# Kernel optimization log

Measured on AMD Instinct MI355X. Metric: run time of the kernel, lower is better.

The kernel has to match this reference:

```python
import jax, jax.numpy as jnp
import numpy as np

IN_FEATURES = 1024
OUT_FEATURES = 1024
NUM_GRIDS = 8
GRID_MIN, GRID_MAX = -2.0, 2.0
DENOM = (GRID_MAX - GRID_MIN) / (NUM_GRIDS - 1)
LN_EPS = 1e-5
GRID = jnp.linspace(GRID_MIN, GRID_MAX, NUM_GRIDS)


def setup_inputs() -> dict:
    key = jax.random.key(0)
    k_x, k_sw, k_bw = jax.random.split(key, 3)
    N = 8192
    x = jax.random.normal(k_x, (N, IN_FEATURES), dtype=jnp.float32)
    ln_gamma = jnp.ones((IN_FEATURES,), dtype=jnp.float32)
    ln_beta = jnp.zeros((IN_FEATURES,), dtype=jnp.float32)
    # trunc_normal(std=0.1) approximated by scaled normal
    spline_w = 0.1 * jax.random.normal(k_sw, (OUT_FEATURES, IN_FEATURES * NUM_GRIDS), dtype=jnp.float32)
    base_w = jax.random.normal(k_bw, (OUT_FEATURES, IN_FEATURES), dtype=jnp.float32) * (1.0 / np.sqrt(IN_FEATURES))
    base_b = jnp.zeros((OUT_FEATURES,), dtype=jnp.float32)
    return {"x": x, "ln_gamma": ln_gamma, "ln_beta": ln_beta,
            "spline_w": spline_w, "base_w": base_w, "base_b": base_b}


def reference(x, ln_gamma, ln_beta, spline_w, base_w, base_b):
    # LayerNorm over last dim
    mu = jnp.mean(x, axis=-1, keepdims=True)
    var = jnp.var(x, axis=-1, keepdims=True)
    xn = (x - mu) * jax.lax.rsqrt(var + LN_EPS) * ln_gamma + ln_beta
    # RBF basis: [N, in, G]
    basis = jnp.exp(-jnp.square((xn[..., None] - GRID) / DENOM))
    basis = basis.reshape(x.shape[0], IN_FEATURES * NUM_GRIDS)
    y = jnp.einsum('nk,ok->no', basis, spline_w)
    y = y + jnp.einsum('nd,od->no', jax.nn.silu(x), base_w) + base_b
    return y
```

## Files before the change

kernel.cpp:

```cpp
#include <hip/hip_runtime.h>
#include <hip/hip_bf16.h>
#include <stdint.h>

#define IN_F 1024
#define OUT_F 1024
#define NG 8
#define KSPLINE 8192
#define KDIM 9216
#define KHALF 4608
#define M_ROWS 8192
#define LOG2E 1.4426950408889634f
#define KC 2.1019642153762872f

#define A_BLOCKS (M_ROWS / 4)
#define W_BLOCKS ((OUT_F * 2304) / 256)
#define RB (KDIM * 2)

using half4v = __attribute__((ext_vector_type(4))) _Float16;
using half8  = __attribute__((ext_vector_type(8))) _Float16;
using f32x4  = __attribute__((ext_vector_type(4))) float;

#define AS1 __attribute__((address_space(1)))
#define AS3 __attribute__((address_space(3)))

__global__ __launch_bounds__(256) void prep_kernel(
        const float* __restrict__ x, const float* __restrict__ gamma,
        const float* __restrict__ beta, const float* __restrict__ sw,
        const float* __restrict__ bw, _Float16* __restrict__ A,
        _Float16* __restrict__ W) {
    if (blockIdx.x >= A_BLOCKS) {
        int idx = (blockIdx.x - A_BLOCKS) * 256 + threadIdx.x;
        int o   = idx / 2304;
        int k4  = idx - o * 2304;
        f32x4 v;
        if (k4 < 2048) v = __builtin_nontemporal_load(&((const f32x4*)sw)[(size_t)o * 2048 + k4]);
        else           v = __builtin_nontemporal_load(&((const f32x4*)bw)[(size_t)o * 256 + (k4 - 2048)]);
        half4v h = { (_Float16)v.x, (_Float16)v.y, (_Float16)v.z, (_Float16)v.w };
        *(half4v*)(W + (size_t)idx * 4) = h;
        return;
    }
    const int wave = threadIdx.x >> 6, lane = threadIdx.x & 63;
    const int row = blockIdx.x * 4 + wave;
    const float* xr = x + (size_t)row * IN_F;

    float xv[16];
    float s = 0.0f, s2 = 0.0f;
#pragma unroll
    for (int j = 0; j < 16; ++j) {
        float v = __builtin_nontemporal_load(&xr[j * 64 + lane]);
        xv[j] = v;
        s += v;
        s2 += v * v;
    }
#pragma unroll
    for (int off = 32; off > 0; off >>= 1) {
        s  += __shfl_xor(s, off);
        s2 += __shfl_xor(s2, off);
    }
    float mu   = s * (1.0f / IN_F);
    float var  = s2 * (1.0f / IN_F) - mu * mu;
    float rstd = rsqrtf(var + 1e-5f);

    const float cq[8] = {
        -2.0000000f * KC, -1.4285715f * KC, -0.8571429f * KC, -0.2857143f * KC,
         0.2857143f * KC,  0.8571429f * KC,  1.4285715f * KC,  2.0000000f * KC };

    _Float16* Arow = A + (size_t)row * KDIM;
    half8* basis_out = (half8*)Arow;
    _Float16* silu_out = Arow + KSPLINE;
#pragma unroll
    for (int j = 0; j < 16; ++j) {
        int f = j * 64 + lane;
        float xs = xv[j];
        float xq = ((xs - mu) * rstd * gamma[f] + beta[f]) * KC;
        half8 h;
#pragma unroll
        for (int g = 0; g < 8; ++g) {
            float v = xq - cq[g];
            h[g] = (_Float16)exp2f(-(v * v));
        }
        __builtin_nontemporal_store(h, &basis_out[f]);
        __builtin_nontemporal_store((_Float16)(xs / (1.0f + exp2f(-xs * LOG2E))), &silu_out[f]);
    }
}

__global__ __launch_bounds__(512, 2) void gemm_kernel(
        const _Float16* __restrict__ A, const _Float16* __restrict__ W,
        const float* __restrict__ bias, float* __restrict__ C,
        float* __restrict__ P, int ntiles, int gpz) {
    extern __shared__ __align__(16) char smem[];
    const int tid  = threadIdx.x;
    const int wave = tid >> 6, lane = tid & 63;
    const int wm = wave >> 2, wn = wave & 3;

    const int lb = blockIdx.x;
    const int per_xcd = gridDim.x >> 5;
    const int xcd = lb & 7, sl = lb >> 3;
    const int g  = xcd * per_xcd + (sl >> 2);
    const int bn = sl & 3;
    const int bm = g / gpz;
    const int z  = g - bm * gpz;

    const int l8 = lane >> 3;
    const int chunkswz = ((lane & 7) ^ l8) << 4;
    const size_t zoff = (size_t)z * (KHALF * 2);
    const int gA[4] = {0, 128, 64, 192};
    const int gB[4] = {0, 128, 32, 160};
    const char* pA[4];
    const char* pB[4];
#pragma unroll
    for (int s = 0; s < 4; ++s) {
        pA[s] = (const char*)A + (size_t)(bm * 256 + gA[s] + wave * 8 + l8) * RB
                + zoff + chunkswz;
        pB[s] = (const char*)W + (size_t)(bn * 256 + gB[s] + (wave >> 2) * 64
                + (wave & 3) * 8 + l8) * RB + zoff + chunkswz;
    }

#define STAGE_A(s, nb, colb) __builtin_amdgcn_global_load_lds( \
        (const AS1 void*)(pA[s] + (colb)), \
        (AS3 void*)(smem + (nb) + (s) * 8192 + wave * 1024), 16, 0, 0)
#define STAGE_B(s, nb, colb) __builtin_amdgcn_global_load_lds( \
        (const AS1 void*)(pB[s] + (colb)), \
        (AS3 void*)(smem + (nb) + 32768 + (s) * 8192 + wave * 1024), 16, 0, 0)

    const int lm  = lane & 15;
    const int hi  = (lane >> 4) << 4;
    const int swz = (lm & 7) << 4;
    const int ck0 = (0  + hi) ^ swz;
    const int ck1 = (64 + hi) ^ swz;
    const int aB0 = (0 + wm) * 8192 + lm * 128;
    const int aB1 = (2 + wm) * 8192 + lm * 128;
    const int bB0 = 32768 + (0 + (wn >> 1)) * 8192 + ((wn & 1) * 32 + lm) * 128;
    const int bB1 = 32768 + (2 + (wn >> 1)) * 8192 + ((wn & 1) * 32 + lm) * 128;

    f32x4 acc[8][4] = {};

    STAGE_A(0, 0, 0); STAGE_A(1, 0, 0);
    STAGE_B(0, 0, 0); STAGE_B(1, 0, 0);
    STAGE_B(2, 0, 0); STAGE_B(3, 0, 0);
    STAGE_A(2, 0, 0); STAGE_A(3, 0, 0);
    asm volatile("s_waitcnt vmcnt(4)" ::: "memory");
    __builtin_amdgcn_s_barrier();

    for (int kt = 0; kt < ntiles; ++kt) {
        const int cb = (kt & 1) * 65536;
        const int nb = cb ^ 65536;
        const size_t col = (size_t)(kt + 1) * 128;
        const bool pref = (kt + 1 < ntiles);

        half8 aF[4][2], bF[2][2];
#pragma unroll
        for (int m = 0; m < 4; ++m) {
            aF[m][0] = *(const half8*)(smem + cb + aB0 + m * 2048 + ck0);
            aF[m][1] = *(const half8*)(smem + cb + aB0 + m * 2048 + ck1);
        }
#pragma unroll
        for (int n = 0; n < 2; ++n) {
            bF[n][0] = *(const half8*)(smem + cb + bB0 + n * 2048 + ck0);
            bF[n][1] = *(const half8*)(smem + cb + bB0 + n * 2048 + ck1);
        }
        asm volatile("s_waitcnt vmcnt(2)" ::: "memory");
        if (pref) { STAGE_A(0, nb, col); STAGE_A(1, nb, col); }
        asm volatile("s_waitcnt lgkmcnt(8)" ::: "memory");
        __builtin_amdgcn_s_barrier();
        asm volatile("s_waitcnt lgkmcnt(0)" ::: "memory");
        __builtin_amdgcn_s_setprio(1);
#pragma unroll
        for (int n = 0; n < 2; ++n)
#pragma unroll
            for (int m = 0; m < 4; ++m)
                acc[m][n] = __builtin_amdgcn_mfma_f32_16x16x32_f16(aF[m][0], bF[n][0], acc[m][n], 0, 0, 0);
#pragma unroll
        for (int n = 0; n < 2; ++n)
#pragma unroll
            for (int m = 0; m < 4; ++m)
                acc[m][n] = __builtin_amdgcn_mfma_f32_16x16x32_f16(aF[m][1], bF[n][1], acc[m][n], 0, 0, 0);
        __builtin_amdgcn_s_setprio(0);
        __builtin_amdgcn_s_barrier();

        half8 bG[2][2];
#pragma unroll
        for (int n = 0; n < 2; ++n) {
            bG[n][0] = *(const half8*)(smem + cb + bB1 + n * 2048 + ck0);
            bG[n][1] = *(const half8*)(smem + cb + bB1 + n * 2048 + ck1);
        }
        if (pref) {
            asm volatile("s_waitcnt vmcnt(2)" ::: "memory");
            STAGE_B(0, nb, col); STAGE_B(1, nb, col);
        } else {
            asm volatile("s_waitcnt vmcnt(0)" ::: "memory");
        }
        __builtin_amdgcn_s_barrier();
        asm volatile("s_waitcnt lgkmcnt(0)" ::: "memory");
        __builtin_amdgcn_s_setprio(1);
#pragma unroll
        for (int n = 0; n < 2; ++n)
#pragma unroll
            for (int m = 0; m < 4; ++m)
                acc[m][2 + n] = __builtin_amdgcn_mfma_f32_16x16x32_f16(aF[m][0], bG[n][0], acc[m][2 + n], 0, 0, 0);
#pragma unroll
        for (int n = 0; n < 2; ++n)
#pragma unroll
            for (int m = 0; m < 4; ++m)
                acc[m][2 + n] = __builtin_amdgcn_mfma_f32_16x16x32_f16(aF[m][1], bG[n][1], acc[m][2 + n], 0, 0, 0);
        __builtin_amdgcn_s_setprio(0);
        __builtin_amdgcn_s_barrier();

        half8 aG[4][2];
#pragma unroll
        for (int m = 0; m < 4; ++m) {
            aG[m][0] = *(const half8*)(smem + cb + aB1 + m * 2048 + ck0);
            aG[m][1] = *(const half8*)(smem + cb + aB1 + m * 2048 + ck1);
        }
        if (pref) { STAGE_B(2, nb, col); STAGE_B(3, nb, col); }
        __builtin_amdgcn_s_barrier();
        asm volatile("s_waitcnt lgkmcnt(0)" ::: "memory");
        __builtin_amdgcn_s_setprio(1);
#pragma unroll
        for (int n = 0; n < 2; ++n)
#pragma unroll
            for (int m = 0; m < 4; ++m)
                acc[4 + m][n] = __builtin_amdgcn_mfma_f32_16x16x32_f16(aG[m][0], bF[n][0], acc[4 + m][n], 0, 0, 0);
#pragma unroll
        for (int n = 0; n < 2; ++n)
#pragma unroll
            for (int m = 0; m < 4; ++m)
                acc[4 + m][n] = __builtin_amdgcn_mfma_f32_16x16x32_f16(aG[m][1], bF[n][1], acc[4 + m][n], 0, 0, 0);
        __builtin_amdgcn_s_setprio(0);
        __builtin_amdgcn_s_barrier();

        if (pref) {
            asm volatile("s_waitcnt vmcnt(2)" ::: "memory");
            STAGE_A(2, nb, col); STAGE_A(3, nb, col);
        }
        __builtin_amdgcn_s_barrier();
        __builtin_amdgcn_s_setprio(1);
#pragma unroll
        for (int n = 0; n < 2; ++n)
#pragma unroll
            for (int m = 0; m < 4; ++m)
                acc[4 + m][2 + n] = __builtin_amdgcn_mfma_f32_16x16x32_f16(aG[m][0], bG[n][0], acc[4 + m][2 + n], 0, 0, 0);
#pragma unroll
        for (int n = 0; n < 2; ++n)
#pragma unroll
            for (int m = 0; m < 4; ++m)
                acc[4 + m][2 + n] = __builtin_amdgcn_mfma_f32_16x16x32_f16(aG[m][1], bG[n][1], acc[4 + m][2 + n], 0, 0, 0);
        __builtin_amdgcn_s_setprio(0);
        __builtin_amdgcn_s_barrier();
    }

    const int cn  = lane & 15;
    const int rm4 = (lane >> 4) * 4;
    float* dst = z ? P : C;
#pragma unroll
    for (int nf = 0; nf < 4; ++nf) {
        int col = bn * 256 + wn * 64 + nf * 16 + cn;
        float bv = z ? 0.0f : bias[col];
#pragma unroll
        for (int mf = 0; mf < 8; ++mf) {
            int row = bm * 256 + wm * 128 + mf * 16 + rm4;
            float* cp = dst + (size_t)row * OUT_F + col;
#pragma unroll
            for (int r = 0; r < 4; ++r)
                cp[(size_t)r * OUT_F] = acc[mf][nf][r] + bv;
        }
    }
}

__global__ __launch_bounds__(256) void reduce_kernel(float* __restrict__ C,
        const float* __restrict__ P) {
    const int n4 = M_ROWS * OUT_F / 4;
    float4* c4 = (float4*)C;
    const float4* p4 = (const float4*)P;
    for (int i = blockIdx.x * 256 + threadIdx.x; i < n4; i += 2048 * 256) {
        float4 a = c4[i];
        float4 b = p4[i];
        a.x += b.x; a.y += b.y; a.z += b.z; a.w += b.w;
        c4[i] = a;
    }
}

extern "C" void kernel_launch(void* const* d_in, const int* in_sizes, int n_in,
                              void* d_out, int out_size, void* d_ws, size_t ws_size,
                              hipStream_t stream) {
    const float* x     = (const float*)d_in[0];
    const float* gamma = (const float*)d_in[1];
    const float* beta  = (const float*)d_in[2];
    const float* sw    = (const float*)d_in[3];
    const float* bw    = (const float*)d_in[4];
    const float* bb    = (const float*)d_in[5];
    float* out = (float*)d_out;

    char* ws = (char*)d_ws;
    size_t offW = 0;
    size_t offA = (size_t)OUT_F * KDIM * 2;
    size_t offP = offA + (size_t)M_ROWS * KDIM * 2;
    size_t need = offP + (size_t)M_ROWS * OUT_F * 4;
    _Float16* Wb = (_Float16*)(ws + offW);
    _Float16* Ab = (_Float16*)(ws + offA);
    float*    Pb = (float*)(ws + offP);
    const int split = (ws_size >= need);

    static int s_attr = 0;
    if (!s_attr) {
        (void)hipFuncSetAttribute(reinterpret_cast<const void*>(gemm_kernel),
                            hipFuncAttributeMaxDynamicSharedMemorySize, 131072);
        s_attr = 1;
    }

    prep_kernel<<<A_BLOCKS + W_BLOCKS, 256, 0, stream>>>(
        x, gamma, beta, sw, bw, Ab, Wb);
    if (split) {
        gemm_kernel<<<256, 512, 131072, stream>>>(Ab, Wb, bb, out, Pb, KHALF / 64, 2);
        reduce_kernel<<<2048, 256, 0, stream>>>(out, Pb);
    } else {
        gemm_kernel<<<128, 512, 131072, stream>>>(Ab, Wb, bb, out, Pb, KDIM / 64, 1);
    }
}
```

Before: 287.5 us.

## Fuse RBF basis generation into GEMM, staging only per-row stats and SiLU

Instead of materializing the 8192x9216 fp16 basis+SiLU matrix in the prep kernel, prep now writes only fp16 SiLU values and per-row mean/rstd. The GEMM kernel computes the eight RBF basis values on the fly from x for the spline K-range and writes them directly into LDS, while still streaming SiLU tiles via global_load_lds for the tail K-range. This removes roughly 150 MB of global write+read traffic for the basis matrix, at the cost of extra exp2 ALU work and fp32 x loads inside the GEMM main loop, and slightly more LDS for gamma/beta.

```diff
diff --git a/kernel.cpp b/kernel.cpp
--- a/kernel.cpp
+++ b/kernel.cpp
@@ -15,19 +15,20 @@
 #define A_BLOCKS (M_ROWS / 4)
 #define W_BLOCKS ((OUT_F * 2304) / 256)
 #define RB (KDIM * 2)
+#define GBOFF 131072
 
 using half4v = __attribute__((ext_vector_type(4))) _Float16;
 using half8  = __attribute__((ext_vector_type(8))) _Float16;
 using f32x4  = __attribute__((ext_vector_type(4))) float;
+using f32x2  = __attribute__((ext_vector_type(2))) float;
 
 #define AS1 __attribute__((address_space(1)))
 #define AS3 __attribute__((address_space(3)))
 
 __global__ __launch_bounds__(256) void prep_kernel(
-        const float* __restrict__ x, const float* __restrict__ gamma,
-        const float* __restrict__ beta, const float* __restrict__ sw,
-        const float* __restrict__ bw, _Float16* __restrict__ A,
-        _Float16* __restrict__ W) {
+        const float* __restrict__ x, const float* __restrict__ sw,
+        const float* __restrict__ bw, _Float16* __restrict__ S,
+        float* __restrict__ musig, _Float16* __restrict__ W) {
     if (blockIdx.x >= A_BLOCKS) {
         int idx = (blockIdx.x - A_BLOCKS) * 256 + threadIdx.x;
         int o   = idx / 2304;
@@ -47,7 +48,7 @@
     float s = 0.0f, s2 = 0.0f;
 #pragma unroll
     for (int j = 0; j < 16; ++j) {
-        float v = __builtin_nontemporal_load(&xr[j * 64 + lane]);
+        float v = xr[j * 64 + lane];
         xv[j] = v;
         s += v;
         s2 += v * v;
@@ -60,32 +61,36 @@
     float mu   = s * (1.0f / IN_F);
     float var  = s2 * (1.0f / IN_F) - mu * mu;
     float rstd = rsqrtf(var + 1e-5f);
-
-    const float cq[8] = {
+    if (lane == 0) {
+        f32x2 ms; ms[0] = mu; ms[1] = rstd;
+        ((f32x2*)musig)[row] = ms;
+    }
+    _Float16* Srow = S + (size_t)row * IN_F;
+#pragma unroll
+    for (int j = 0; j < 16; ++j) {
+        float xs = xv[j];
+        Srow[j * 64 + lane] = (_Float16)(xs / (1.0f + exp2f(-xs * LOG2E)));
+    }
+}
+
+__device__ __forceinline__ half8 spline8(float xv, float mu, float rs, float gk, float bk) {
+    const float cqg[8] = {
         -2.0000000f * KC, -1.4285715f * KC, -0.8571429f * KC, -0.2857143f * KC,
          0.2857143f * KC,  0.8571429f * KC,  1.4285715f * KC,  2.0000000f * KC };
-
-    _Float16* Arow = A + (size_t)row * KDIM;
-    half8* basis_out = (half8*)Arow;
-    _Float16* silu_out = Arow + KSPLINE;
-#pragma unroll
-    for (int j = 0; j < 16; ++j) {
-        int f = j * 64 + lane;
-        float xs = xv[j];
-        float xq = ((xs - mu) * rstd * gamma[f] + beta[f]) * KC;
-        half8 h;
-#pragma unroll
-        for (int g = 0; g < 8; ++g) {
-            float v = xq - cq[g];
-            h[g] = (_Float16)exp2f(-(v * v));
-        }
-        __builtin_nontemporal_store(h, &basis_out[f]);
-        __builtin_nontemporal_store((_Float16)(xs / (1.0f + exp2f(-xs * LOG2E))), &silu_out[f]);
-    }
+    float xq = fmaf((xv - mu) * rs, gk, bk);
+    half8 h;
+#pragma unroll
+    for (int g = 0; g < 8; ++g) {
+        float d = xq - cqg[g];
+        h[g] = (_Float16)__builtin_amdgcn_exp2f(-(d * d));
+    }
+    return h;
 }
 
 __global__ __launch_bounds__(512, 2) void gemm_kernel(
-        const _Float16* __restrict__ A, const _Float16* __restrict__ W,
+        const _Float16* __restrict__ W, const _Float16* __restrict__ S,
+        const float* __restrict__ x, const float* __restrict__ musig,
+        const float* __restrict__ gamma, const float* __restrict__ beta,
         const float* __restrict__ bias, float* __restrict__ C,
         float* __restrict__ P, int ntiles, int gpz) {
     extern __shared__ __align__(16) char smem[];
@@ -100,28 +105,40 @@
     const int bn = sl & 3;
     const int bm = g / gpz;
     const int z  = g - bm * gpz;
+    const int ksoff = z * KHALF;
 
     const int l8 = lane >> 3;
     const int chunkswz = ((lane & 7) ^ l8) << 4;
-    const size_t zoff = (size_t)z * (KHALF * 2);
-    const int gA[4] = {0, 128, 64, 192};
-    const int gB[4] = {0, 128, 32, 160};
-    const char* pA[4];
+    const int gAr[4] = {0, 128, 64, 192};
+    const int gB[4]  = {0, 128, 32, 160};
     const char* pB[4];
+    const char* pS[4];
+    const float* xp[4];
 #pragma unroll
     for (int s = 0; s < 4; ++s) {
-        pA[s] = (const char*)A + (size_t)(bm * 256 + gA[s] + wave * 8 + l8) * RB
-                + zoff + chunkswz;
         pB[s] = (const char*)W + (size_t)(bn * 256 + gB[s] + (wave >> 2) * 64
-                + (wave & 3) * 8 + l8) * RB + zoff + chunkswz;
-    }
-
-#define STAGE_A(s, nb, colb) __builtin_amdgcn_global_load_lds( \
-        (const AS1 void*)(pA[s] + (colb)), \
-        (AS3 void*)(smem + (nb) + (s) * 8192 + wave * 1024), 16, 0, 0)
+                + (wave & 3) * 8 + l8) * RB + (size_t)ksoff * 2 + chunkswz;
+        int arow = bm * 256 + gAr[s] + wave * 8 + l8;
+        pS[s] = (const char*)S + (size_t)arow * (IN_F * 2) + chunkswz;
+    }
+    const int r6 = tid >> 3;
+    const int c8 = tid & 7;
+    const int wAbase = r6 * 128 + ((c8 ^ (r6 & 7)) << 4);
+    float mu4[4], rs4[4];
+#pragma unroll
+    for (int s = 0; s < 4; ++s) {
+        int arow = bm * 256 + gAr[s] + r6;
+        xp[s] = x + (size_t)arow * IN_F;
+        f32x2 ms = ((const f32x2*)musig)[arow];
+        mu4[s] = ms[0]; rs4[s] = ms[1];
+    }
+
 #define STAGE_B(s, nb, colb) __builtin_amdgcn_global_load_lds( \
         (const AS1 void*)(pB[s] + (colb)), \
         (AS3 void*)(smem + (nb) + 32768 + (s) * 8192 + wave * 1024), 16, 0, 0)
+#define STAGE_S(s, nb, colb) __builtin_amdgcn_global_load_lds( \
+        (const AS1 void*)(pS[s] + (colb)), \
+        (AS3 void*)(smem + (nb) + (s) * 8192 + wave * 1024), 16, 0, 0)
 
     const int lm  = lane & 15;
     const int hi  = (lane >> 4) << 4;
@@ -135,19 +152,68 @@
 
     f32x4 acc[8][4] = {};
 
-    STAGE_A(0, 0, 0); STAGE_A(1, 0, 0);
-    STAGE_B(0, 0, 0); STAGE_B(1, 0, 0);
-    STAGE_B(2, 0, 0); STAGE_B(3, 0, 0);
-    STAGE_A(2, 0, 0); STAGE_A(3, 0, 0);
-    asm volatile("s_waitcnt vmcnt(4)" ::: "memory");
+#define MFMA_QUAD(MB, NB2, Aa, Bb)                                              \
+    __builtin_amdgcn_s_barrier();                                               \
+    asm volatile("s_waitcnt lgkmcnt(0)" ::: "memory");                          \
+    __builtin_amdgcn_sched_barrier(0);                                          \
+    __builtin_amdgcn_s_setprio(1);                                              \
+    _Pragma("unroll")                                                           \
+    for (int n = 0; n < 2; ++n)                                                 \
+        _Pragma("unroll")                                                       \
+        for (int m = 0; m < 4; ++m)                                             \
+            acc[(MB)+m][(NB2)+n] = __builtin_amdgcn_mfma_f32_16x16x32_f16(      \
+                Aa[m][0], Bb[n][0], acc[(MB)+m][(NB2)+n], 0, 0, 0);             \
+    _Pragma("unroll")                                                           \
+    for (int n = 0; n < 2; ++n)                                                 \
+        _Pragma("unroll")                                                       \
+        for (int m = 0; m < 4; ++m)                                             \
+            acc[(MB)+m][(NB2)+n] = __builtin_amdgcn_mfma_f32_16x16x32_f16(      \
+                Aa[m][1], Bb[n][1], acc[(MB)+m][(NB2)+n], 0, 0, 0);             \
+    __builtin_amdgcn_s_setprio(0);                                              \
+    __builtin_amdgcn_s_barrier();
+
+    {
+        f32x2 t0; t0[0] = gamma[tid] * KC;       t0[1] = beta[tid] * KC;
+        f32x2 t1; t1[0] = gamma[tid + 512] * KC; t1[1] = beta[tid + 512] * KC;
+        *(f32x2*)(smem + GBOFF + tid * 8) = t0;
+        *(f32x2*)(smem + GBOFF + (tid + 512) * 8) = t1;
+    }
+    const int f00 = z * 576 + c8;
+    float xf0[4];
+#pragma unroll
+    for (int s = 0; s < 4; ++s) xf0[s] = xp[s][f00];
+    STAGE_B(0, 0, 0); STAGE_B(1, 0, 0); STAGE_B(2, 0, 0); STAGE_B(3, 0, 0);
+    __syncthreads();
+    {
+        f32x2 gb0 = *(const f32x2*)(smem + GBOFF + f00 * 8);
+#pragma unroll
+        for (int s = 0; s < 4; ++s) {
+            half8 h = spline8(xf0[s], mu4[s], rs4[s], gb0[0], gb0[1]);
+            *(half8*)(smem + s * 8192 + wAbase) = h;
+        }
+    }
+    asm volatile("s_waitcnt lgkmcnt(0)" ::: "memory");
     __builtin_amdgcn_s_barrier();
 
     for (int kt = 0; kt < ntiles; ++kt) {
         const int cb = (kt & 1) * 65536;
         const int nb = cb ^ 65536;
-        const size_t col = (size_t)(kt + 1) * 128;
         const bool pref = (kt + 1 < ntiles);
-
+        const int nk = ksoff + (kt + 1) * 64;
+        const bool nsil = nk >= KSPLINE;
+        const size_t bcolb = (size_t)(kt + 1) * 128;
+        const int fb = z * 576 + (kt + 1) * 8 + c8;
+        size_t scolb = 0;
+        if (nsil) scolb = (size_t)(nk - KSPLINE) * 2;
+
+        float xf[4];
+        if (pref) {
+            if (nsil) { STAGE_S(0, nb, scolb); STAGE_S(1, nb, scolb); }
+            else {
+#pragma unroll
+                for (int s = 0; s < 4; ++s) xf[s] = xp[s][fb];
+            }
+        }
         half8 aF[4][2], bF[2][2];
 #pragma unroll
         for (int m = 0; m < 4; ++m) {
@@ -159,24 +225,14 @@
             bF[n][0] = *(const half8*)(smem + cb + bB0 + n * 2048 + ck0);
             bF[n][1] = *(const half8*)(smem + cb + bB0 + n * 2048 + ck1);
         }
-        asm volatile("s_waitcnt vmcnt(2)" ::: "memory");
-        if (pref) { STAGE_A(0, nb, col); STAGE_A(1, nb, col); }
+        if (pref) {
+            if (nsil) asm volatile("s_waitcnt vmcnt(2)" ::: "memory");
+            else      asm volatile("s_waitcnt vmcnt(4)" ::: "memory");
+        } else {
+            asm volatile("s_waitcnt vmcnt(0)" ::: "memory");
+        }
         asm volatile("s_waitcnt lgkmcnt(8)" ::: "memory");
-        __builtin_amdgcn_s_barrier();
-        asm volatile("s_waitcnt lgkmcnt(0)" ::: "memory");
-        __builtin_amdgcn_s_setprio(1);
-#pragma unroll
-        for (int n = 0; n < 2; ++n)
-#pragma unroll
-            for (int m = 0; m < 4; ++m)
-                acc[m][n] = __builtin_amdgcn_mfma_f32_16x16x32_f16(aF[m][0], bF[n][0], acc[m][n], 0, 0, 0);
-#pragma unroll
-        for (int n = 0; n < 2; ++n)
-#pragma unroll
-            for (int m = 0; m < 4; ++m)
-                acc[m][n] = __builtin_amdgcn_mfma_f32_16x16x32_f16(aF[m][1], bF[n][1], acc[m][n], 0, 0, 0);
-        __builtin_amdgcn_s_setprio(0);
-        __builtin_amdgcn_s_barrier();
+        MFMA_QUAD(0, 0, aF, bF)
 
         half8 bG[2][2];
 #pragma unroll
@@ -184,27 +240,8 @@
             bG[n][0] = *(const half8*)(smem + cb + bB1 + n * 2048 + ck0);
             bG[n][1] = *(const half8*)(smem + cb + bB1 + n * 2048 + ck1);
         }
-        if (pref) {
-            asm volatile("s_waitcnt vmcnt(2)" ::: "memory");
-            STAGE_B(0, nb, col); STAGE_B(1, nb, col);
-        } else {
-            asm volatile("s_waitcnt vmcnt(0)" ::: "memory");
-        }
-        __builtin_amdgcn_s_barrier();
-        asm volatile("s_waitcnt lgkmcnt(0)" ::: "memory");
-        __builtin_amdgcn_s_setprio(1);
-#pragma unroll
-        for (int n = 0; n < 2; ++n)
-#pragma unroll
-            for (int m = 0; m < 4; ++m)
-                acc[m][2 + n] = __builtin_amdgcn_mfma_f32_16x16x32_f16(aF[m][0], bG[n][0], acc[m][2 + n], 0, 0, 0);
-#pragma unroll
-        for (int n = 0; n < 2; ++n)
-#pragma unroll
-            for (int m = 0; m < 4; ++m)
-                acc[m][2 + n] = __builtin_amdgcn_mfma_f32_16x16x32_f16(aF[m][1], bG[n][1], acc[m][2 + n], 0, 0, 0);
-        __builtin_amdgcn_s_setprio(0);
-        __builtin_amdgcn_s_barrier();
+        if (pref) { STAGE_B(0, nb, bcolb); STAGE_B(1, nb, bcolb); }
+        MFMA_QUAD(0, 2, aF, bG)
 
         half8 aG[4][2];
 #pragma unroll
@@ -212,41 +249,33 @@
             aG[m][0] = *(const half8*)(smem + cb + aB1 + m * 2048 + ck0);
             aG[m][1] = *(const half8*)(smem + cb + aB1 + m * 2048 + ck1);
         }
-        if (pref) { STAGE_B(2, nb, col); STAGE_B(3, nb, col); }
-        __builtin_amdgcn_s_barrier();
+        f32x2 gb;
+        if (pref) {
+            if (!nsil) {
+                gb = *(const f32x2*)(smem + GBOFF + fb * 8);
+                half8 h0 = spline8(xf[0], mu4[0], rs4[0], gb[0], gb[1]);
+                half8 h1 = spline8(xf[1], mu4[1], rs4[1], gb[0], gb[1]);
+                *(half8*)(smem + nb + 0 * 8192 + wAbase) = h0;
+                *(half8*)(smem + nb + 1 * 8192 + wAbase) = h1;
+            }
+            STAGE_B(2, nb, bcolb); STAGE_B(3, nb, bcolb);
+        }
+        MFMA_QUAD(4, 0, aG, bF)
+
+        if (pref) {
+            if (!nsil) {
+                half8 h2 = spline8(xf[2], mu4[2], rs4[2], gb[0], gb[1]);
+                half8 h3 = spline8(xf[3], mu4[3], rs4[3], gb[0], gb[1]);
+                *(half8*)(smem + nb + 2 * 8192 + wAbase) = h2;
+                *(half8*)(smem + nb + 3 * 8192 + wAbase) = h3;
+            }
+            asm volatile("s_waitcnt vmcnt(2)" ::: "memory");
+            if (nsil) { STAGE_S(2, nb, scolb); STAGE_S(3, nb, scolb); }
+        } else {
+            asm volatile("s_waitcnt vmcnt(0)" ::: "memory");
+        }
         asm volatile("s_waitcnt lgkmcnt(0)" ::: "memory");
-        __builtin_amdgcn_s_setprio(1);
-#pragma unroll
-        for (int n = 0; n < 2; ++n)
-#pragma unroll
-            for (int m = 0; m < 4; ++m)
-                acc[4 + m][n] = __builtin_amdgcn_mfma_f32_16x16x32_f16(aG[m][0], bF[n][0], acc[4 + m][n], 0, 0, 0);
-#pragma unroll
-        for (int n = 0; n < 2; ++n)
-#pragma unroll
-            for (int m = 0; m < 4; ++m)
-                acc[4 + m][n] = __builtin_amdgcn_mfma_f32_16x16x32_f16(aG[m][1], bF[n][1], acc[4 + m][n], 0, 0, 0);
-        __builtin_amdgcn_s_setprio(0);
-        __builtin_amdgcn_s_barrier();
-
-        if (pref) {
-            asm volatile("s_waitcnt vmcnt(2)" ::: "memory");
-            STAGE_A(2, nb, col); STAGE_A(3, nb, col);
-        }
-        __builtin_amdgcn_s_barrier();
-        __builtin_amdgcn_s_setprio(1);
-#pragma unroll
-        for (int n = 0; n < 2; ++n)
-#pragma unroll
-            for (int m = 0; m < 4; ++m)
-                acc[4 + m][2 + n] = __builtin_amdgcn_mfma_f32_16x16x32_f16(aG[m][0], bG[n][0], acc[4 + m][2 + n], 0, 0, 0);
-#pragma unroll
-        for (int n = 0; n < 2; ++n)
-#pragma unroll
-            for (int m = 0; m < 4; ++m)
-                acc[4 + m][2 + n] = __builtin_amdgcn_mfma_f32_16x16x32_f16(aG[m][1], bG[n][1], acc[4 + m][2 + n], 0, 0, 0);
-        __builtin_amdgcn_s_setprio(0);
-        __builtin_amdgcn_s_barrier();
+        MFMA_QUAD(4, 2, aG, bG)
     }
 
     const int cn  = lane & 15;
@@ -293,27 +322,31 @@
 
     char* ws = (char*)d_ws;
     size_t offW = 0;
-    size_t offA = (size_t)OUT_F * KDIM * 2;
-    size_t offP = offA + (size_t)M_ROWS * KDIM * 2;
+    size_t offS = (size_t)OUT_F * KDIM * 2;
+    size_t offM = offS + (size_t)M_ROWS * IN_F * 2;
+    size_t offP = offM + (size_t)M_ROWS * 8;
     size_t need = offP + (size_t)M_ROWS * OUT_F * 4;
     _Float16* Wb = (_Float16*)(ws + offW);
-    _Float16* Ab = (_Float16*)(ws + offA);
+    _Float16* Sb = (_Float16*)(ws + offS);
+    float*    Mb = (float*)(ws + offM);
     float*    Pb = (float*)(ws + offP);
     const int split = (ws_size >= need);
 
     static int s_attr = 0;
     if (!s_attr) {
         (void)hipFuncSetAttribute(reinterpret_cast<const void*>(gemm_kernel),
-                            hipFuncAttributeMaxDynamicSharedMemorySize, 131072);
+                            hipFuncAttributeMaxDynamicSharedMemorySize, 139264);
         s_attr = 1;
     }
 
     prep_kernel<<<A_BLOCKS + W_BLOCKS, 256, 0, stream>>>(
-        x, gamma, beta, sw, bw, Ab, Wb);
+        x, sw, bw, Sb, Mb, Wb);
     if (split) {
-        gemm_kernel<<<256, 512, 131072, stream>>>(Ab, Wb, bb, out, Pb, KHALF / 64, 2);
+        gemm_kernel<<<256, 512, 139264, stream>>>(
+            Wb, Sb, x, Mb, gamma, beta, bb, out, Pb, KHALF / 64, 2);
         reduce_kernel<<<2048, 256, 0, stream>>>(out, Pb);
     } else {
-        gemm_kernel<<<128, 512, 131072, stream>>>(Ab, Wb, bb, out, Pb, KDIM / 64, 1);
-    }
-}
+        gemm_kernel<<<128, 512, 139264, stream>>>(
+            Wb, Sb, x, Mb, gamma, beta, bb, out, Pb, KDIM / 64, 1);
+    }
+}
```

New measurement: 315.3 us. 1.1x slower.

## Compute RBF basis via exponential recurrence and vectorize prep with permuted K layout

Applied to the files above, without the earlier changes.

The prep kernel now evaluates the eight Gaussian basis values with two exp2 calls and a multiplicative recurrence instead of eight exp2 calls. It loads x, gamma and beta as float4 and writes silu as half4. The spline K dimension is permuted consistently in both A and W, so the vectorized writes stay coalesced and the GEMM result is unchanged. The recurrence can lose a little accuracy in fp16 for far-off grid points, and the prep kernel is a small part of total time next to the GEMM.

```diff
diff --git a/kernel.cpp b/kernel.cpp
--- a/kernel.cpp
+++ b/kernel.cpp
@@ -11,9 +11,15 @@
 #define M_ROWS 8192
 #define LOG2E 1.4426950408889634f
 #define KC 2.1019642153762872f
+#define CQ0 (-2.0f * KC)
+#define DQ  (0.5714285714285714f * KC)
+#define DQ2 1.4426950408889634f
+#define QCHAIN 0.1353352832366127f
+
 
 #define A_BLOCKS (M_ROWS / 4)
-#define W_BLOCKS ((OUT_F * 2304) / 256)
+#define WS_BLOCKS 4096
+#define WSIL_BLOCKS 1024
 #define RB (KDIM * 2)
 
 using half4v = __attribute__((ext_vector_type(4))) _Float16;
@@ -22,35 +28,58 @@
 
 #define AS1 __attribute__((address_space(1)))
 #define AS3 __attribute__((address_space(3)))
+
+__device__ __forceinline__ half8 spline8c(float xq) {
+    float d0 = xq - CQ0;
+    float b  = __builtin_amdgcn_exp2f(-(d0 * d0));
+    float r  = __builtin_amdgcn_exp2f(fmaf(2.0f * DQ, d0, -DQ2));
+    half8 h;
+#pragma unroll
+    for (int g = 0; g < 8; ++g) {
+        h[g] = (_Float16)b;
+        if (g < 7) { b = b * r; r = r * QCHAIN; }
+    }
+    return h;
+}
 
 __global__ __launch_bounds__(256) void prep_kernel(
         const float* __restrict__ x, const float* __restrict__ gamma,
         const float* __restrict__ beta, const float* __restrict__ sw,
         const float* __restrict__ bw, _Float16* __restrict__ A,
         _Float16* __restrict__ W) {
-    if (blockIdx.x >= A_BLOCKS) {
-        int idx = (blockIdx.x - A_BLOCKS) * 256 + threadIdx.x;
-        int o   = idx / 2304;
-        int k4  = idx - o * 2304;
-        f32x4 v;
-        if (k4 < 2048) v = __builtin_nontemporal_load(&((const f32x4*)sw)[(size_t)o * 2048 + k4]);
-        else           v = __builtin_nontemporal_load(&((const f32x4*)bw)[(size_t)o * 256 + (k4 - 2048)]);
+    const int b = blockIdx.x;
+    if (b >= A_BLOCKS + WS_BLOCKS) {
+        int t = (b - A_BLOCKS - WS_BLOCKS) * 256 + threadIdx.x;
+        int o = t >> 8, d4 = t & 255;
+        f32x4 v = __builtin_nontemporal_load(&((const f32x4*)bw)[o * 256 + d4]);
         half4v h = { (_Float16)v.x, (_Float16)v.y, (_Float16)v.z, (_Float16)v.w };
-        *(half4v*)(W + (size_t)idx * 4) = h;
+        *(half4v*)(W + (size_t)o * KDIM + KSPLINE + d4 * 4) = h;
         return;
     }
+    if (b >= A_BLOCKS) {
+        int t = (b - A_BLOCKS) * 256 + threadIdx.x;
+        int o = t >> 10, f = t & 1023;
+        const f32x4* src = &((const f32x4*)sw)[((size_t)o * 1024 + f) * 2];
+        f32x4 v0 = __builtin_nontemporal_load(src);
+        f32x4 v1 = __builtin_nontemporal_load(src + 1);
+        half8 h = { (_Float16)v0.x, (_Float16)v0.y, (_Float16)v0.z, (_Float16)v0.w,
+                    (_Float16)v1.x, (_Float16)v1.y, (_Float16)v1.z, (_Float16)v1.w };
+        int p8 = (f >> 8) * 256 + (f & 3) * 64 + ((f >> 2) & 63);
+        *(half8*)(W + (size_t)o * KDIM + p8 * 8) = h;
+        return;
+    }
     const int wave = threadIdx.x >> 6, lane = threadIdx.x & 63;
-    const int row = blockIdx.x * 4 + wave;
-    const float* xr = x + (size_t)row * IN_F;
-
-    float xv[16];
+    const int row = b * 4 + wave;
+    const f32x4* xr4 = (const f32x4*)(x + (size_t)row * IN_F);
+
+    f32x4 xv[4];
     float s = 0.0f, s2 = 0.0f;
 #pragma unroll
-    for (int j = 0; j < 16; ++j) {
-        float v = __builtin_nontemporal_load(&xr[j * 64 + lane]);
+    for (int j = 0; j < 4; ++j) {
+        f32x4 v = xr4[j * 64 + lane];
         xv[j] = v;
-        s += v;
-        s2 += v * v;
+        s  += v.x + v.y + v.z + v.w;
+        s2 += v.x * v.x + v.y * v.y + v.z * v.z + v.w * v.w;
     }
 #pragma unroll
     for (int off = 32; off > 0; off >>= 1) {
@@ -61,26 +90,26 @@
     float var  = s2 * (1.0f / IN_F) - mu * mu;
     float rstd = rsqrtf(var + 1e-5f);
 
-    const float cq[8] = {
-        -2.0000000f * KC, -1.4285715f * KC, -0.8571429f * KC, -0.2857143f * KC,
-         0.2857143f * KC,  0.8571429f * KC,  1.4285715f * KC,  2.0000000f * KC };
-
     _Float16* Arow = A + (size_t)row * KDIM;
-    half8* basis_out = (half8*)Arow;
     _Float16* silu_out = Arow + KSPLINE;
 #pragma unroll
-    for (int j = 0; j < 16; ++j) {
-        int f = j * 64 + lane;
-        float xs = xv[j];
-        float xq = ((xs - mu) * rstd * gamma[f] + beta[f]) * KC;
-        half8 h;
-#pragma unroll
-        for (int g = 0; g < 8; ++g) {
-            float v = xq - cq[g];
-            h[g] = (_Float16)exp2f(-(v * v));
-        }
-        __builtin_nontemporal_store(h, &basis_out[f]);
-        __builtin_nontemporal_store((_Float16)(xs / (1.0f + exp2f(-xs * LOG2E))), &silu_out[f]);
+    for (int j = 0; j < 4; ++j) {
+        int idx = j * 64 + lane;
+        f32x4 g  = ((const f32x4*)gamma)[idx];
+        f32x4 bt = ((const f32x4*)beta)[idx];
+        float xs4[4] = { xv[j].x, xv[j].y, xv[j].z, xv[j].w };
+        float gg[4]  = { g.x, g.y, g.z, g.w };
+        float bb4[4] = { bt.x, bt.y, bt.z, bt.w };
+        half4v sil;
+#pragma unroll
+        for (int c = 0; c < 4; ++c) {
+            float xs = xs4[c];
+            float xq = fmaf((xs - mu) * rstd, gg[c] * KC, bb4[c] * KC);
+            half8 h = spline8c(xq);
+            *(half8*)(Arow + (size_t)(j * 256 + c * 64 + lane) * 8) = h;
+            sil[c] = (_Float16)(xs / (1.0f + exp2f(-xs * LOG2E)));
+        }
+        *(half4v*)(silu_out + idx * 4) = sil;
     }
 }
 
@@ -308,7 +337,7 @@
         s_attr = 1;
     }
 
-    prep_kernel<<<A_BLOCKS + W_BLOCKS, 256, 0, stream>>>(
+    prep_kernel<<<A_BLOCKS + WS_BLOCKS + WSIL_BLOCKS, 256, 0, stream>>>(
         x, gamma, beta, sw, bw, Ab, Wb);
     if (split) {
         gemm_kernel<<<256, 512, 131072, stream>>>(Ab, Wb, bb, out, Pb, KHALF / 64, 2);
```

Result: no change. 285.9 us (-0.6%).
